# Kernel optimization log

Measured on AMD Instinct MI355X. Metric: run time of the kernel, lower is better.

Reference implementation:

```python
import jax, jax.numpy as jnp
import numpy as np

N_NODES = 100000
N_EDGES = 1600000
D_IN = 128
D_HID = 128
D_OUT = 128


def _sage_conv(x, src, dst, W_l, b_l, W_r, num_nodes):
    # PyG SAGEConv (aggr='mean'): out = lin_l(mean_{j in N(i)} x_j) + lin_r(x_i)
    msg = x[src]  # [E, d] gather source features
    agg = jax.ops.segment_sum(msg, dst, num_segments=num_nodes)  # [N, d]
    deg = jax.ops.segment_sum(jnp.ones((src.shape[0],), x.dtype), dst, num_segments=num_nodes)
    mean = agg / jnp.maximum(deg, 1.0)[:, None]
    return mean @ W_l.T + b_l + x @ W_r.T


def setup_inputs() -> dict:
    key = jax.random.key(0)
    ks = jax.random.split(key, 8)
    x = jax.random.normal(ks[0], (N_NODES, D_IN), dtype=jnp.float32)
    edge_index = jax.random.randint(ks[1], (2, N_EDGES), 0, N_NODES, dtype=jnp.int64)
    s = 1.0 / np.sqrt(D_IN)
    W_l1 = jax.random.uniform(ks[2], (D_HID, D_IN), jnp.float32, -s, s)
    b_l1 = jnp.zeros((D_HID,), jnp.float32)
    W_r1 = jax.random.uniform(ks[3], (D_HID, D_IN), jnp.float32, -s, s)
    s2 = 1.0 / np.sqrt(D_HID)
    W_l2 = jax.random.uniform(ks[4], (D_OUT, D_HID), jnp.float32, -s2, s2)
    b_l2 = jnp.zeros((D_OUT,), jnp.float32)
    W_r2 = jax.random.uniform(ks[5], (D_OUT, D_HID), jnp.float32, -s2, s2)
    return {"x": x, "edge_index": edge_index, "W_l1": W_l1, "b_l1": b_l1,
            "W_r1": W_r1, "W_l2": W_l2, "b_l2": b_l2, "W_r2": W_r2}


def reference(x, edge_index, W_l1, b_l1, W_r1, W_l2, b_l2, W_r2):
    src, dst = edge_index[0], edge_index[1]
    n = x.shape[0]
    h = _sage_conv(x, src, dst, W_l1, b_l1, W_r1, n)
    h = jax.nn.relu(h)
    out = _sage_conv(h, src, dst, W_l2, b_l2, W_r2, n)
    return out
```

## Files before the change

### kernel.cpp

```cpp
#include <hip/hip_runtime.h>
#include <stdint.h>

typedef short bf16x8 __attribute__((ext_vector_type(8)));
typedef unsigned short u16x8 __attribute__((ext_vector_type(8)));
typedef float f32x4 __attribute__((ext_vector_type(4)));

#define NPB 512
#define BSHIFT 9
#define MAXBUCK 256
#define STAGE_CAP 12288
#define LROW 136

__device__ __forceinline__ short f2bf(float f) {
    uint32_t u = __float_as_uint(f);
    u += 0x7fffu + ((u >> 16) & 1u);
    return (short)(u >> 16);
}
__device__ __forceinline__ float bf2f(unsigned short s) {
    return __uint_as_float((uint32_t)s << 16);
}

__global__ __launch_bounds__(256) void convx_kernel(const float* __restrict__ in,
                                                    short* __restrict__ out, int n) {
    int i = (blockIdx.x * 256 + threadIdx.x) * 8;
    if (i + 8 <= n) {
        const float4 v0 = *(const float4*)(in + i);
        const float4 v1 = *(const float4*)(in + i + 4);
        bf16x8 o;
        o[0] = f2bf(v0.x); o[1] = f2bf(v0.y); o[2] = f2bf(v0.z); o[3] = f2bf(v0.w);
        o[4] = f2bf(v1.x); o[5] = f2bf(v1.y); o[6] = f2bf(v1.z); o[7] = f2bf(v1.w);
        *(bf16x8*)(out + i) = o;
    } else {
        for (int j = i; j < n; ++j) out[j] = f2bf(in[j]);
    }
}

__global__ void convw4_kernel(const float* __restrict__ w0, const float* __restrict__ w1,
                              const float* __restrict__ w2, const float* __restrict__ w3,
                              short* __restrict__ o0, short* __restrict__ o1,
                              short* __restrict__ o2, short* __restrict__ o3) {
    int i = blockIdx.x * 256 + threadIdx.x;
    o0[i] = f2bf(w0[i]);
    o1[i] = f2bf(w1[i]);
    o2[i] = f2bf(w2[i]);
    o3[i] = f2bf(w3[i]);
}

__global__ __launch_bounds__(256) void bhist_kernel(const int* __restrict__ dst,
                                                    int* __restrict__ bcnt, int E, int B) {
    __shared__ int h[MAXBUCK];
    for (int i = threadIdx.x; i < B; i += 256) h[i] = 0;
    __syncthreads();
    int stride = gridDim.x * 256;
    for (int e = blockIdx.x * 256 + threadIdx.x; e < E; e += stride)
        atomicAdd(&h[dst[e] >> BSHIFT], 1);
    __syncthreads();
    for (int i = threadIdx.x; i < B; i += 256)
        if (h[i]) atomicAdd(&bcnt[i], h[i]);
}

__global__ __launch_bounds__(256) void bscan_kernel(const int* __restrict__ bcnt,
                                                    int* __restrict__ bbase,
                                                    int* __restrict__ gcur,
                                                    int* __restrict__ rowptr,
                                                    int E, int N, int B) {
    __shared__ int s[256];
    int t = threadIdx.x;
    int v = (t < B) ? bcnt[t] : 0;
    s[t] = v;
    __syncthreads();
    for (int off = 1; off < 256; off <<= 1) {
        int a = (t >= off) ? s[t - off] : 0;
        __syncthreads();
        s[t] += a;
        __syncthreads();
    }
    int excl = s[t] - v;
    if (t < B) { bbase[t] = excl; gcur[t] = excl; }
    if (t == B - 1) bbase[B] = excl + v;
    if (t == 0) rowptr[N] = E;
}

__global__ __launch_bounds__(256) void bin_kernel(const int* __restrict__ src,
                                                  const int* __restrict__ dst,
                                                  int* __restrict__ gcur,
                                                  unsigned int* __restrict__ binned,
                                                  int E, int B) {
    __shared__ int cnt[MAXBUCK];
    __shared__ int base[MAXBUCK];
    for (int i = threadIdx.x; i < B; i += 256) cnt[i] = 0;
    __syncthreads();
    const int e0 = blockIdx.x * 4096;
    int myS[16], myD[16];
    int n = 0;
#pragma unroll
    for (int i = 0; i < 16; ++i) {
        int e = e0 + threadIdx.x + i * 256;
        if (e < E) { myS[n] = src[e]; myD[n] = dst[e]; ++n; }
    }
    for (int i = 0; i < n; ++i) atomicAdd(&cnt[myD[i] >> BSHIFT], 1);
    __syncthreads();
    for (int i = threadIdx.x; i < B; i += 256) {
        int c = cnt[i];
        base[i] = c ? atomicAdd(&gcur[i], c) : 0;
        cnt[i] = 0;
    }
    __syncthreads();
    for (int i = 0; i < n; ++i) {
        int b = myD[i] >> BSHIFT;
        int off = atomicAdd(&cnt[b], 1);
        binned[base[b] + off] = ((unsigned)myS[i] << BSHIFT) | (unsigned)(myD[i] & (NPB - 1));
    }
}

__global__ __launch_bounds__(256) void build_kernel(const unsigned int* __restrict__ binned,
                                                    const int* __restrict__ bbase,
                                                    int* __restrict__ rowptr,
                                                    int* __restrict__ csr, int N) {
    __shared__ int hist[NPB];
    __shared__ int cur[NPB];
    __shared__ int scanb[256];
    __shared__ int stage[STAGE_CAP];
    const int b = blockIdx.x;
    const int t = threadIdx.x;
    const int cbeg = bbase[b], cend = bbase[b + 1];
    const int cnt = cend - cbeg;
    for (int i = t; i < NPB; i += 256) hist[i] = 0;
    __syncthreads();
    for (int i = t; i < cnt; i += 256)
        atomicAdd(&hist[binned[cbeg + i] & (NPB - 1)], 1);
    __syncthreads();
    const int h0 = hist[2 * t], h1 = hist[2 * t + 1];
    const int ps = h0 + h1;
    scanb[t] = ps;
    __syncthreads();
    for (int off = 1; off < 256; off <<= 1) {
        int a = (t >= off) ? scanb[t - off] : 0;
        __syncthreads();
        scanb[t] += a;
        __syncthreads();
    }
    const int e0 = scanb[t] - ps;
    cur[2 * t]     = e0;
    cur[2 * t + 1] = e0 + h0;
    __syncthreads();
    const int node0 = b << BSHIFT;
    for (int i = t; i < NPB; i += 256) {
        int node = node0 + i;
        if (node < N) rowptr[node] = cbeg + cur[i];
    }
    __syncthreads();
    for (int i = t; i < cnt; i += 256) {
        unsigned rec = binned[cbeg + i];
        int ld  = rec & (NPB - 1);
        int pos = atomicAdd(&cur[ld], 1);
        if (pos < STAGE_CAP) stage[pos] = (int)(rec >> BSHIFT);
        else                 csr[cbeg + pos] = (int)(rec >> BSHIFT);
    }
    __syncthreads();
    const int lim = cnt < STAGE_CAP ? cnt : STAGE_CAP;
    for (int i = t; i < lim; i += 256)
        csr[cbeg + i] = stage[i];
}

template <bool RELU>
__global__ __launch_bounds__(256) void fused_kernel(
    const short* __restrict__ feat, const int* __restrict__ csr,
    const int* __restrict__ rowptr,
    const short* __restrict__ Wl, const short* __restrict__ Wr,
    const float* __restrict__ bias,
    short* __restrict__ outb, float* __restrict__ outf, int N)
{
    __shared__ short lmean[64 * LROW];
    const int lane = threadIdx.x & 63;
    const int wave = threadIdx.x >> 6;
    const int q    = lane >> 4;
    const int ql   = lane & 15;
    const int m0   = blockIdx.x * 64 + wave * 16;

    for (int it = 0; it < 4; ++it) {
        const int node = m0 + it * 4 + q;
        float a0=0,a1=0,a2=0,a3=0,a4=0,a5=0,a6=0,a7=0;
        if (node < N) {
            const int beg = rowptr[node], end = rowptr[node + 1];
            int e = beg;
            for (; e + 4 <= end; e += 4) {
                const int s0 = csr[e], s1 = csr[e+1], s2 = csr[e+2], s3 = csr[e+3];
                u16x8 u0 = *(const u16x8*)(feat + (size_t)s0 * 128 + ql * 8);
                u16x8 u1 = *(const u16x8*)(feat + (size_t)s1 * 128 + ql * 8);
                u16x8 u2 = *(const u16x8*)(feat + (size_t)s2 * 128 + ql * 8);
                u16x8 u3 = *(const u16x8*)(feat + (size_t)s3 * 128 + ql * 8);
                a0 += bf2f(u0[0]) + bf2f(u1[0]) + bf2f(u2[0]) + bf2f(u3[0]);
                a1 += bf2f(u0[1]) + bf2f(u1[1]) + bf2f(u2[1]) + bf2f(u3[1]);
                a2 += bf2f(u0[2]) + bf2f(u1[2]) + bf2f(u2[2]) + bf2f(u3[2]);
                a3 += bf2f(u0[3]) + bf2f(u1[3]) + bf2f(u2[3]) + bf2f(u3[3]);
                a4 += bf2f(u0[4]) + bf2f(u1[4]) + bf2f(u2[4]) + bf2f(u3[4]);
                a5 += bf2f(u0[5]) + bf2f(u1[5]) + bf2f(u2[5]) + bf2f(u3[5]);
                a6 += bf2f(u0[6]) + bf2f(u1[6]) + bf2f(u2[6]) + bf2f(u3[6]);
                a7 += bf2f(u0[7]) + bf2f(u1[7]) + bf2f(u2[7]) + bf2f(u3[7]);
            }
            for (; e < end; ++e) {
                u16x8 u = *(const u16x8*)(feat + (size_t)csr[e] * 128 + ql * 8);
                a0 += bf2f(u[0]); a1 += bf2f(u[1]); a2 += bf2f(u[2]); a3 += bf2f(u[3]);
                a4 += bf2f(u[4]); a5 += bf2f(u[5]); a6 += bf2f(u[6]); a7 += bf2f(u[7]);
            }
            const float r = 1.0f / fmaxf((float)(end - beg), 1.0f);
            bf16x8 o;
            o[0] = f2bf(a0 * r); o[1] = f2bf(a1 * r); o[2] = f2bf(a2 * r); o[3] = f2bf(a3 * r);
            o[4] = f2bf(a4 * r); o[5] = f2bf(a5 * r); o[6] = f2bf(a6 * r); o[7] = f2bf(a7 * r);
            *(bf16x8*)(lmean + (size_t)(wave * 16 + it * 4 + q) * LROW + ql * 8) = o;
        }
    }

    f32x4 acc[8];
#pragma unroll
    for (int i = 0; i < 8; ++i) acc[i] = (f32x4)0.0f;
    const bool valid = (m0 + ql < N);

#pragma unroll
    for (int kk = 0; kk < 4; ++kk) {
        const int kb = kk * 32 + q * 8;
        const bf16x8 a = *(const bf16x8*)(lmean + (size_t)(wave * 16 + ql) * LROW + kb);
#pragma unroll
        for (int nt = 0; nt < 8; ++nt) {
            const bf16x8 b = *(const bf16x8*)(Wl + (size_t)(nt * 16 + ql) * 128 + kb);
            acc[nt] = __builtin_amdgcn_mfma_f32_16x16x32_bf16(a, b, acc[nt], 0, 0, 0);
        }
    }
#pragma unroll
    for (int kk = 0; kk < 4; ++kk) {
        const int kb = kk * 32 + q * 8;
        bf16x8 a = (bf16x8)0;
        if (valid) a = *(const bf16x8*)(feat + (size_t)(m0 + ql) * 128 + kb);
#pragma unroll
        for (int nt = 0; nt < 8; ++nt) {
            const bf16x8 b = *(const bf16x8*)(Wr + (size_t)(nt * 16 + ql) * 128 + kb);
            acc[nt] = __builtin_amdgcn_mfma_f32_16x16x32_bf16(a, b, acc[nt], 0, 0, 0);
        }
    }

    const int rbase = m0 + q * 4;
#pragma unroll
    for (int nt = 0; nt < 8; ++nt) {
        const int col = nt * 16 + ql;
        const float bc = bias[col];
#pragma unroll
        for (int r = 0; r < 4; ++r) {
            const int node = rbase + r;
            if (node < N) {
                float v = acc[nt][r] + bc;
                if (RELU) outb[(size_t)node * 128 + col] = f2bf(fmaxf(v, 0.0f));
                else      outf[(size_t)node * 128 + col] = v;
            }
        }
    }
}

extern "C" void kernel_launch(void* const* d_in, const int* in_sizes, int n_in,
                              void* d_out, int out_size, void* d_ws, size_t ws_size,
                              hipStream_t stream) {
    const float* x   = (const float*)d_in[0];
    const int*   ei  = (const int*)d_in[1];
    const float* Wl1 = (const float*)d_in[2];
    const float* bl1 = (const float*)d_in[3];
    const float* Wr1 = (const float*)d_in[4];
    const float* Wl2 = (const float*)d_in[5];
    const float* bl2 = (const float*)d_in[6];
    const float* Wr2 = (const float*)d_in[7];

    const int N = in_sizes[0] / 128;
    const int E = in_sizes[1] / 2;
    const int* src = ei;
    const int* dst = ei + E;
    const int B = (N + NPB - 1) >> BSHIFT;

    char* wsb = (char*)d_ws;
    short* hbuf = (short*)wsb;
    size_t off = (size_t)N * 128 * 2;
    short* wl1 = (short*)(wsb + off); off += 16384 * 2;
    short* wr1 = (short*)(wsb + off); off += 16384 * 2;
    short* wl2 = (short*)(wsb + off); off += 16384 * 2;
    short* wr2 = (short*)(wsb + off); off += 16384 * 2;
    int* rowptr = (int*)(wsb + off);
    off += ((size_t)(N + 1) * 4 + 15) & ~(size_t)15;
    int* csr = (int*)(wsb + off);
    off += ((size_t)E * 4 + 15) & ~(size_t)15;
    unsigned int* binned = (unsigned int*)(wsb + off);
    off += ((size_t)E * 4 + 15) & ~(size_t)15;
    int* bcnt  = (int*)(wsb + off);
    int* bbase = bcnt + (MAXBUCK + 1);
    int* gcur  = bbase + (MAXBUCK + 1);

    short* xb  = (short*)d_out;
    float* out = (float*)d_out;

    const int fusedBlocks = (N + 63) / 64;
    const int binBlocks   = (E + 4095) / 4096;

    convx_kernel<<<(N * 128 / 8 + 255) / 256, 256, 0, stream>>>(x, xb, N * 128);
    convw4_kernel<<<64, 256, 0, stream>>>(Wl1, Wr1, Wl2, Wr2, wl1, wr1, wl2, wr2);

    (void)hipMemsetAsync(bcnt, 0, (size_t)(MAXBUCK + 1) * sizeof(int), stream);
    bhist_kernel<<<256, 256, 0, stream>>>(dst, bcnt, E, B);
    bscan_kernel<<<1, 256, 0, stream>>>(bcnt, bbase, gcur, rowptr, E, N, B);
    bin_kernel<<<binBlocks, 256, 0, stream>>>(src, dst, gcur, binned, E, B);
    build_kernel<<<B, 256, 0, stream>>>(binned, bbase, rowptr, csr, N);

    fused_kernel<true><<<fusedBlocks, 256, 0, stream>>>(xb, csr, rowptr, wl1, wr1, bl1,
                                                        hbuf, (float*)nullptr, N);
    fused_kernel<false><<<fusedBlocks, 256, 0, stream>>>(hbuf, csr, rowptr, wl2, wr2, bl2,
                                                         (short*)nullptr, out, N);
}
```

Before: 432.9 us.

## Aggregate one node per wave with edge-parallel gather and shuffle reduction

The mean-aggregation phase now handles one node at a time per wave. It loads up to 64 CSR indices with a single coalesced read and broadcasts them by shuffle. Each quarter-wave gathers a different neighbor row, and the partial sums are combined with xor shuffles. Previously each quarter-wave walked a different node's edge list, which unbalanced work when degrees differ and made the index loads serial. The bin kernel also gets fixed-trip unrolled loops that use sentinel values instead of a compacted count, so its arrays can stay in registers. The trade-off is 16 serial node iterations per wave plus the extra shuffle-reduction cost.

```diff
diff --git a/kernel.cpp b/kernel.cpp
--- a/kernel.cpp
+++ b/kernel.cpp
@@ -92,13 +92,16 @@
     __syncthreads();
     const int e0 = blockIdx.x * 4096;
     int myS[16], myD[16];
-    int n = 0;
 #pragma unroll
     for (int i = 0; i < 16; ++i) {
         int e = e0 + threadIdx.x + i * 256;
-        if (e < E) { myS[n] = src[e]; myD[n] = dst[e]; ++n; }
-    }
-    for (int i = 0; i < n; ++i) atomicAdd(&cnt[myD[i] >> BSHIFT], 1);
+        bool v = e < E;
+        myS[i] = v ? src[e] : 0;
+        myD[i] = v ? dst[e] : -1;
+    }
+#pragma unroll
+    for (int i = 0; i < 16; ++i)
+        if (myD[i] >= 0) atomicAdd(&cnt[myD[i] >> BSHIFT], 1);
     __syncthreads();
     for (int i = threadIdx.x; i < B; i += 256) {
         int c = cnt[i];
@@ -106,10 +109,13 @@
         cnt[i] = 0;
     }
     __syncthreads();
-    for (int i = 0; i < n; ++i) {
-        int b = myD[i] >> BSHIFT;
-        int off = atomicAdd(&cnt[b], 1);
-        binned[base[b] + off] = ((unsigned)myS[i] << BSHIFT) | (unsigned)(myD[i] & (NPB - 1));
+#pragma unroll
+    for (int i = 0; i < 16; ++i) {
+        if (myD[i] >= 0) {
+            int b = myD[i] >> BSHIFT;
+            int off = atomicAdd(&cnt[b], 1);
+            binned[base[b] + off] = ((unsigned)myS[i] << BSHIFT) | (unsigned)(myD[i] & (NPB - 1));
+        }
     }
 }
 
@@ -178,37 +184,44 @@
     const int ql   = lane & 15;
     const int m0   = blockIdx.x * 64 + wave * 16;
 
-    for (int it = 0; it < 4; ++it) {
-        const int node = m0 + it * 4 + q;
+    for (int n = 0; n < 16; ++n) {
+        const int node = m0 + n;
+        if (node >= N) break;
+        const int beg = rowptr[node], end = rowptr[node + 1];
         float a0=0,a1=0,a2=0,a3=0,a4=0,a5=0,a6=0,a7=0;
-        if (node < N) {
-            const int beg = rowptr[node], end = rowptr[node + 1];
-            int e = beg;
-            for (; e + 4 <= end; e += 4) {
-                const int s0 = csr[e], s1 = csr[e+1], s2 = csr[e+2], s3 = csr[e+3];
-                u16x8 u0 = *(const u16x8*)(feat + (size_t)s0 * 128 + ql * 8);
-                u16x8 u1 = *(const u16x8*)(feat + (size_t)s1 * 128 + ql * 8);
-                u16x8 u2 = *(const u16x8*)(feat + (size_t)s2 * 128 + ql * 8);
-                u16x8 u3 = *(const u16x8*)(feat + (size_t)s3 * 128 + ql * 8);
-                a0 += bf2f(u0[0]) + bf2f(u1[0]) + bf2f(u2[0]) + bf2f(u3[0]);
-                a1 += bf2f(u0[1]) + bf2f(u1[1]) + bf2f(u2[1]) + bf2f(u3[1]);
-                a2 += bf2f(u0[2]) + bf2f(u1[2]) + bf2f(u2[2]) + bf2f(u3[2]);
-                a3 += bf2f(u0[3]) + bf2f(u1[3]) + bf2f(u2[3]) + bf2f(u3[3]);
-                a4 += bf2f(u0[4]) + bf2f(u1[4]) + bf2f(u2[4]) + bf2f(u3[4]);
-                a5 += bf2f(u0[5]) + bf2f(u1[5]) + bf2f(u2[5]) + bf2f(u3[5]);
-                a6 += bf2f(u0[6]) + bf2f(u1[6]) + bf2f(u2[6]) + bf2f(u3[6]);
-                a7 += bf2f(u0[7]) + bf2f(u1[7]) + bf2f(u2[7]) + bf2f(u3[7]);
+        int base = beg;
+        while (base < end) {
+            const int cnt = min(end - base, 64);
+            const int idx = (lane < cnt) ? csr[base + lane] : 0;
+            for (int it = 0; it * 4 < cnt; ++it) {
+                const int sel = it * 4 + q;
+                const int s = __shfl(idx, sel);
+                if (sel < cnt) {
+                    u16x8 u = *(const u16x8*)(feat + (size_t)s * 128 + ql * 8);
+                    a0 += bf2f(u[0]); a1 += bf2f(u[1]);
+                    a2 += bf2f(u[2]); a3 += bf2f(u[3]);
+                    a4 += bf2f(u[4]); a5 += bf2f(u[5]);
+                    a6 += bf2f(u[6]); a7 += bf2f(u[7]);
+                }
             }
-            for (; e < end; ++e) {
-                u16x8 u = *(const u16x8*)(feat + (size_t)csr[e] * 128 + ql * 8);
-                a0 += bf2f(u[0]); a1 += bf2f(u[1]); a2 += bf2f(u[2]); a3 += bf2f(u[3]);
-                a4 += bf2f(u[4]); a5 += bf2f(u[5]); a6 += bf2f(u[6]); a7 += bf2f(u[7]);
-            }
+            base += 64;
+        }
+        a0 += __shfl_xor(a0, 16); a1 += __shfl_xor(a1, 16);
+        a2 += __shfl_xor(a2, 16); a3 += __shfl_xor(a3, 16);
+        a4 += __shfl_xor(a4, 16); a5 += __shfl_xor(a5, 16);
+        a6 += __shfl_xor(a6, 16); a7 += __shfl_xor(a7, 16);
+        a0 += __shfl_xor(a0, 32); a1 += __shfl_xor(a1, 32);
+        a2 += __shfl_xor(a2, 32); a3 += __shfl_xor(a3, 32);
+        a4 += __shfl_xor(a4, 32); a5 += __shfl_xor(a5, 32);
+        a6 += __shfl_xor(a6, 32); a7 += __shfl_xor(a7, 32);
+        if (q == 0) {
             const float r = 1.0f / fmaxf((float)(end - beg), 1.0f);
             bf16x8 o;
-            o[0] = f2bf(a0 * r); o[1] = f2bf(a1 * r); o[2] = f2bf(a2 * r); o[3] = f2bf(a3 * r);
-            o[4] = f2bf(a4 * r); o[5] = f2bf(a5 * r); o[6] = f2bf(a6 * r); o[7] = f2bf(a7 * r);
-            *(bf16x8*)(lmean + (size_t)(wave * 16 + it * 4 + q) * LROW + ql * 8) = o;
+            o[0] = f2bf(a0 * r); o[1] = f2bf(a1 * r);
+            o[2] = f2bf(a2 * r); o[3] = f2bf(a3 * r);
+            o[4] = f2bf(a4 * r); o[5] = f2bf(a5 * r);
+            o[6] = f2bf(a6 * r); o[7] = f2bf(a7 * r);
+            *(bf16x8*)(lmean + (size_t)(wave * 16 + n) * LROW + ql * 8) = o;
         }
     }
 
```

Measured after the change: 481.1 us. 1.11x slower.
